# Kernel optimization log

Measured on AMD Instinct MI355X. Metric: run time of the kernel, lower is better.

## Reference

```python
import jax, jax.numpy as jnp
import numpy as np

N, E, DIN, DOUT = 30000, 480000, 512, 512


def setup_inputs() -> dict:
    key = jax.random.key(0)
    ks = jax.random.split(key, 20)
    inp = {}
    inp["x"] = jax.random.normal(ks[0], (N, DIN), jnp.float32)
    inp["edge_index"] = jax.random.randint(ks[1], (2, E), 0, N, dtype=jnp.int64)
    inp["edge_weight"] = jax.random.uniform(ks[2], (E,), jnp.float32)
    sc = 1.0 / np.sqrt(DIN)
    sl = 1.0 / np.sqrt(2 * DOUT)
    for i, g in enumerate(["i", "f", "g", "o"]):
        inp[f"Wc_{g}"] = jax.random.normal(ks[3 + 4 * i], (DIN, DOUT), jnp.float32) * sc
        inp[f"bc_{g}"] = jnp.zeros((DOUT,), jnp.float32)
        inp[f"Wl_{g}"] = jax.random.normal(ks[4 + 4 * i], (2 * DOUT, DOUT), jnp.float32) * sl
        inp[f"bl_{g}"] = jnp.zeros((DOUT,), jnp.float32)
    return inp


def _gcn_norm(src, dst, w, n):
    # add self loops with weight 1.0 (improved=False), then symmetric normalization
    loops = jnp.arange(n, dtype=src.dtype)
    src = jnp.concatenate([src, loops])
    dst = jnp.concatenate([dst, loops])
    w = jnp.concatenate([w, jnp.ones((n,), w.dtype)])
    deg = jax.ops.segment_sum(w, dst, num_segments=n)
    dinv = jnp.where(deg > 0, jax.lax.rsqrt(jnp.where(deg > 0, deg, 1.0)), 0.0)
    norm = dinv[src] * w * dinv[dst]
    return src, dst, norm


def reference(x, edge_index, edge_weight,
              Wc_i, bc_i, Wl_i, bl_i,
              Wc_f, bc_f, Wl_f, bl_f,
              Wc_g, bc_g, Wl_g, bl_g,
              Wc_o, bc_o, Wl_o, bl_o):
    n = x.shape[0]
    src, dst, norm = _gcn_norm(edge_index[0], edge_index[1], edge_weight, n)
    H = jnp.zeros((n, DOUT), x.dtype)  # _set_hidden_state default
    C = jnp.zeros((n, DOUT), x.dtype)  # _set_cell_state default

    def conv(Wc, bc):
        xw = x @ Wc                                        # [N, DOUT] dense GEMM
        agg = jax.ops.segment_sum(norm[:, None] * xw[src], dst, num_segments=n)
        return agg + bc

    def gate(Wc, bc, Wl, bl, act):
        z = jnp.concatenate([conv(Wc, bc), H], axis=1)      # [N, 2*DOUT]
        return act(z @ Wl + bl)

    I = gate(Wc_i, bc_i, Wl_i, bl_i, jax.nn.sigmoid)
    F = gate(Wc_f, bc_f, Wl_f, bl_f, jax.nn.sigmoid)
    G = gate(Wc_g, bc_g, Wl_g, bl_g, jnp.tanh)
    O = gate(Wc_o, bc_o, Wl_o, bl_o, jax.nn.sigmoid)
    Cn = F * C + I * G
    Hn = O * jnp.tanh(Cn)
    return O, Hn, Cn
```

## Files before the change

### kernel.cpp

```cpp
#include <hip/hip_runtime.h>
#include <stdint.h>

typedef __bf16 bf16;
typedef __attribute__((ext_vector_type(4))) float f4;
typedef __attribute__((ext_vector_type(4))) float f32x4;
typedef __attribute__((ext_vector_type(8))) __bf16 bf8v;
typedef __attribute__((ext_vector_type(4))) __bf16 bf4v;

#define NN 30000
#define MPAD 30080
#define OUTSTRIDE 15360000

typedef __attribute__((address_space(3))) unsigned int as3_u32;
typedef __attribute__((address_space(1))) unsigned int as1_u32;

__device__ __forceinline__ void gl_lds16(const void* g, void* l) {
  __builtin_amdgcn_global_load_lds((as1_u32*)g, (as3_u32*)l, 16, 0, 0);
}

__global__ void k_init(float* deg, int* counts, int* cursor, int n) {
  int i = blockIdx.x * 256 + threadIdx.x;
  if (i < n) { deg[i] = 1.0f; counts[i] = 0; cursor[i] = 0; }
}

__global__ void k_pre(const int* __restrict__ ei, const float* __restrict__ ew,
                      float* __restrict__ deg, int* __restrict__ counts, int E) {
  int e = blockIdx.x * 256 + threadIdx.x;
  if (e < E) {
    int d = ei[E + e];
    atomicAdd(&deg[d], ew[e]);
    atomicAdd(&counts[d], 1);
  }
}

__global__ void k_dinv(float* dinv, int n) {
  int i = blockIdx.x * 256 + threadIdx.x;
  if (i < n) { float d = dinv[i]; dinv[i] = d > 0.f ? rsqrtf(d) : 0.f; }
}

__global__ void k_bsum(const int* __restrict__ counts, int* __restrict__ bsum, int n) {
  __shared__ int sm[256];
  int i = blockIdx.x * 256 + threadIdx.x;
  sm[threadIdx.x] = (i < n) ? counts[i] : 0;
  __syncthreads();
  for (int st = 128; st > 0; st >>= 1) {
    if (threadIdx.x < st) sm[threadIdx.x] += sm[threadIdx.x + st];
    __syncthreads();
  }
  if (threadIdx.x == 0) bsum[blockIdx.x] = sm[0];
}

__global__ void k_bscan(int* bsum, int nb) {
  __shared__ int buf[128];
  int t = threadIdx.x;
  int v = (t < nb) ? bsum[t] : 0;
  buf[t] = v;
  __syncthreads();
  for (int s = 1; s < 128; s <<= 1) {
    int u = (t >= s) ? buf[t - s] : 0;
    __syncthreads();
    buf[t] += u;
    __syncthreads();
  }
  if (t < nb) bsum[t] = buf[t] - v;
}

__global__ void k_offs(const int* __restrict__ counts, const int* __restrict__ bsum,
                       int* __restrict__ offs, int n, int E) {
  __shared__ int buf[256];
  int i = blockIdx.x * 256 + threadIdx.x;
  int v = (i < n) ? counts[i] : 0;
  buf[threadIdx.x] = v;
  __syncthreads();
  for (int s = 1; s < 256; s <<= 1) {
    int u = (threadIdx.x >= s) ? buf[threadIdx.x - s] : 0;
    __syncthreads();
    buf[threadIdx.x] += u;
    __syncthreads();
  }
  if (i < n) offs[i] = bsum[blockIdx.x] + buf[threadIdx.x] - v;
  if (i == 0) offs[n] = E;
}

__global__ void k_scatter(const int* __restrict__ ei, const float* __restrict__ ew,
                          const float* __restrict__ dinv, const int* __restrict__ offs,
                          int* __restrict__ cursor, int* __restrict__ srcs,
                          float* __restrict__ norms, int E) {
  int e = blockIdx.x * 256 + threadIdx.x;
  if (e >= E) return;
  int s = ei[e], d = ei[E + e];
  int pos = offs[d] + atomicAdd(&cursor[d], 1);
  srcs[pos] = s;
  norms[pos] = dinv[s] * ew[e] * dinv[d];
}

__global__ void k_xbf(const float* __restrict__ x, bf16* __restrict__ xbf, int n8) {
  int i = blockIdx.x * 256 + threadIdx.x;
  if (i >= n8) return;
  const f4* x4 = (const f4*)x;
  f4 a = x4[2 * i], b = x4[2 * i + 1];
  bf8v o;
#pragma unroll
  for (int j = 0; j < 4; ++j) { o[j] = (bf16)a[j]; o[4 + j] = (bf16)b[j]; }
  ((bf8v*)xbf)[i] = o;
}

__global__ __launch_bounds__(256) void k_agg(const int* __restrict__ offs, const int* __restrict__ srcs,
                                             const float* __restrict__ norms, const float* __restrict__ x,
                                             const float* __restrict__ dinv, const bf16* __restrict__ xbf,
                                             bf16* __restrict__ ybf) {
  int wv = (blockIdx.x * 256 + threadIdx.x) >> 6;
  int lane = threadIdx.x & 63;
  if (wv >= MPAD) return;
  bf16* yrow = ybf + ((size_t)wv << 9) + lane * 8;
  if (wv >= NN) {
    bf8v z;
#pragma unroll
    for (int j = 0; j < 8; ++j) z[j] = (bf16)0.f;
    *(bf8v*)yrow = z;
    return;
  }
  float acc[8];
  float s0 = dinv[wv]; s0 *= s0;
  const f4* xr = (const f4*)(x + ((size_t)wv << 9)) + lane * 2;
  f4 a = xr[0], b = xr[1];
#pragma unroll
  for (int j = 0; j < 4; ++j) { acc[j] = s0 * a[j]; acc[4 + j] = s0 * b[j]; }
  int e = offs[wv], end = offs[wv + 1];
  for (; e + 2 <= end; e += 2) {
    int s1 = srcs[e], s2 = srcs[e + 1];
    float n1 = norms[e], n2 = norms[e + 1];
    bf8v v1 = *(const bf8v*)(xbf + ((size_t)s1 << 9) + lane * 8);
    bf8v v2 = *(const bf8v*)(xbf + ((size_t)s2 << 9) + lane * 8);
#pragma unroll
    for (int j = 0; j < 8; ++j) acc[j] += n1 * (float)v1[j] + n2 * (float)v2[j];
  }
  if (e < end) {
    int s1 = srcs[e]; float n1 = norms[e];
    bf8v v1 = *(const bf8v*)(xbf + ((size_t)s1 << 9) + lane * 8);
#pragma unroll
    for (int j = 0; j < 8; ++j) acc[j] += n1 * (float)v1[j];
  }
  bf8v o;
#pragma unroll
  for (int j = 0; j < 8; ++j) o[j] = (bf16)acc[j];
  *(bf8v*)yrow = o;
}

__global__ void k_wcomb(const float* __restrict__ WcA, const float* __restrict__ WlA,
                        const float* __restrict__ WcB, const float* __restrict__ WlB,
                        const float* __restrict__ WcC, const float* __restrict__ WlC,
                        bf16* __restrict__ Wt) {
  const float* Wc; const float* Wl;
  int g = blockIdx.z;
  if (g == 0)      { Wc = WcA; Wl = WlA; }
  else if (g == 1) { Wc = WcB; Wl = WlB; }
  else             { Wc = WcC; Wl = WlC; }
  int k0 = blockIdx.x * 64, j0 = blockIdx.y * 64;
  int t = threadIdx.x, tx = t & 15, ty = t >> 4;
  __shared__ float sWc[64][17];
  __shared__ float sWl[16][64];
  float acc[4][4] = {};
  for (int c0 = 0; c0 < 512; c0 += 16) {
    { int kk = t >> 2, c4 = (t & 3) * 4;
      f4 v = *(const f4*)(Wc + (size_t)(k0 + kk) * 512 + c0 + c4);
#pragma unroll
      for (int j = 0; j < 4; ++j) sWc[kk][c4 + j] = v[j]; }
    { int cc = t >> 4, j4 = (t & 15) * 4;
      f4 v = *(const f4*)(Wl + (size_t)(c0 + cc) * 512 + j0 + j4);
      *(f4*)&sWl[cc][j4] = v; }
    __syncthreads();
#pragma unroll
    for (int cc = 0; cc < 16; ++cc) {
      float wcv[4], wlv[4];
#pragma unroll
      for (int b = 0; b < 4; ++b) wcv[b] = sWc[tx * 4 + b][cc];
#pragma unroll
      for (int a = 0; a < 4; ++a) wlv[a] = sWl[cc][ty * 4 + a];
#pragma unroll
      for (int a = 0; a < 4; ++a)
#pragma unroll
        for (int b = 0; b < 4; ++b) acc[a][b] += wlv[a] * wcv[b];
    }
    __syncthreads();
  }
#pragma unroll
  for (int a = 0; a < 4; ++a) {
    bf4v o;
#pragma unroll
    for (int b = 0; b < 4; ++b) o[b] = (bf16)acc[a][b];
    *(bf4v*)&Wt[((size_t)g * 512 + j0 + ty * 4 + a) * 512 + k0 + tx * 4] = o;
  }
}

__global__ void k_bcomb3(const float* __restrict__ bcA, const float* __restrict__ blA, const float* __restrict__ WlA,
                         const float* __restrict__ bcB, const float* __restrict__ blB, const float* __restrict__ WlB,
                         const float* __restrict__ bcC, const float* __restrict__ blC, const float* __restrict__ WlC,
                         float* __restrict__ bcomb) {
  int g = blockIdx.x >> 3, jc = blockIdx.x & 7;
  const float* bc; const float* bl; const float* Wl;
  if (g == 0)      { bc = bcA; bl = blA; Wl = WlA; }
  else if (g == 1) { bc = bcB; bl = blB; Wl = WlB; }
  else             { bc = bcC; bl = blC; Wl = WlC; }
  int jl = threadIdx.x & 63, part = threadIdx.x >> 6;
  int j = jc * 64 + jl;
  float s = 0.f;
  for (int c = part * 128; c < part * 128 + 128; ++c)
    s += bc[c] * Wl[(size_t)c * 512 + j];
  __shared__ float sm[4][64];
  sm[part][jl] = s;
  __syncthreads();
  if (part == 0)
    bcomb[g * 512 + j] = bl[j] + sm[0][jl] + sm[1][jl] + sm[2][jl] + sm[3][jl];
}

__global__ __launch_bounds__(256) void k_gemm(const bf16* __restrict__ A, const bf16* __restrict__ Bt,
                                              const float* __restrict__ bcomb, float* __restrict__ out) {
  __shared__ __align__(16) char lds[81920];
  const int t = threadIdx.x, lane = t & 63, w = t >> 6;
  const int wm = w >> 1, wn = w & 1;
  const int d = blockIdx.x;
  const int s = (d & 7) * 235 + (d >> 3);
  const int m0 = (s >> 3) * 128, n0 = (s & 7) * 64;
  const int l15 = lane & 15, lhi = lane >> 4;
  f32x4 acc[3][4][2] = {};

  auto stage = [&](char* base, int ks) {
    const int k0b = ks * 128;
#pragma unroll
    for (int it = 0; it < 4; ++it) {
      int P = (((it * 4 + w) << 6) | lane) << 4;
      int r = P >> 7;
      int wl = (P & 127) ^ ((r & 7) << 4);
      gl_lds16((const char*)A + (((size_t)(m0 + r)) << 10) + k0b + wl, base + P);
    }
#pragma unroll
    for (int it = 0; it < 6; ++it) {
      int flat = it * 4 + w;
      int g = flat >> 3, q = flat & 7;
      int P = ((q << 6) | lane) << 4;
      int n = P >> 7;
      int wl = (P & 127) ^ ((n & 7) << 4);
      gl_lds16((const char*)Bt + (((size_t)(g * 512 + n0 + n)) << 10) + k0b + wl,
               base + 16384 + g * 8192 + P);
    }
  };

  auto compute = [&](const char* base) {
#pragma unroll
    for (int kh = 0; kh < 2; ++kh) {
      bf8v af[4];
#pragma unroll
      for (int mi = 0; mi < 4; ++mi) {
        int r = wm * 64 + mi * 16 + l15;
        int off = (kh * 64 + lhi * 16) ^ ((r & 7) << 4);
        af[mi] = *(const bf8v*)(base + r * 128 + off);
      }
      bf8v bfr[3][2];
#pragma unroll
      for (int g = 0; g < 3; ++g)
#pragma unroll
        for (int ni = 0; ni < 2; ++ni) {
          int n = wn * 32 + ni * 16 + l15;
          int off = (kh * 64 + lhi * 16) ^ ((n & 7) << 4);
          bfr[g][ni] = *(const bf8v*)(base + 16384 + g * 8192 + n * 128 + off);
        }
#pragma unroll
      for (int g = 0; g < 3; ++g)
#pragma unroll
        for (int mi = 0; mi < 4; ++mi)
#pragma unroll
          for (int ni = 0; ni < 2; ++ni)
            acc[g][mi][ni] = __builtin_amdgcn_mfma_f32_16x16x32_bf16(bfr[g][ni], af[mi], acc[g][mi][ni], 0, 0, 0);
    }
  };

  stage(lds, 0);
  __syncthreads();
#pragma unroll
  for (int kp = 0; kp < 4; ++kp) {
    stage(lds + 40960, 2 * kp + 1);
    compute(lds);
    __syncthreads();
    if (kp < 3) stage(lds, 2 * kp + 2);
    compute(lds + 40960);
    __syncthreads();
  }

#pragma unroll
  for (int ni = 0; ni < 2; ++ni) {
    int nb = n0 + wn * 32 + ni * 16 + lhi * 4;
    f4 bI = *(const f4*)&bcomb[nb];
    f4 bG = *(const f4*)&bcomb[512 + nb];
    f4 bO = *(const f4*)&bcomb[1024 + nb];
#pragma unroll
    for (int mi = 0; mi < 4; ++mi) {
      int row = m0 + wm * 64 + mi * 16 + l15;
      if (row < NN) {
        f4 vO, vH, vC;
#pragma unroll
        for (int r = 0; r < 4; ++r) {
          float zi = acc[0][mi][ni][r] + bI[r];
          float zg = acc[1][mi][ni][r] + bG[r];
          float zo = acc[2][mi][ni][r] + bO[r];
          float I = 1.f / (1.f + __expf(-zi));
          float e2g = __expf(2.f * zg);
          float G = (e2g - 1.f) / (e2g + 1.f);
          float O = 1.f / (1.f + __expf(-zo));
          float Cn = I * G;
          float e2c = __expf(2.f * Cn);
          float tc = (e2c - 1.f) / (e2c + 1.f);
          vO[r] = O; vH[r] = O * tc; vC[r] = Cn;
        }
        size_t base = ((size_t)row << 9) + nb;
        *(f4*)&out[base] = vO;
        *(f4*)&out[OUTSTRIDE + base] = vH;
        *(f4*)&out[2 * OUTSTRIDE + base] = vC;
      }
    }
  }
}

extern "C" void kernel_launch(void* const* d_in, const int* in_sizes, int n_in,
                              void* d_out, int out_size, void* d_ws, size_t ws_size,
                              hipStream_t stream) {
  const float* x   = (const float*)d_in[0];
  const int*   ei  = (const int*)d_in[1];
  const float* ew  = (const float*)d_in[2];
  const float* Wc_i = (const float*)d_in[3];
  const float* bc_i = (const float*)d_in[4];
  const float* Wl_i = (const float*)d_in[5];
  const float* bl_i = (const float*)d_in[6];
  const float* Wc_g = (const float*)d_in[11];
  const float* bc_g = (const float*)d_in[12];
  const float* Wl_g = (const float*)d_in[13];
  const float* bl_g = (const float*)d_in[14];
  const float* Wc_o = (const float*)d_in[15];
  const float* bc_o = (const float*)d_in[16];
  const float* Wl_o = (const float*)d_in[17];
  const float* bl_o = (const float*)d_in[18];

  const int E = in_sizes[2];
  const int n = in_sizes[0] / 512;
  const int NB = (n + 255) / 256;

  char* ws = (char*)d_ws;
  bf16*  ybf   = (bf16*)ws;
  float* dinv  = (float*)(ws + 30801920);
  bf16*  Wt    = (bf16*)(ws + 30924800);
  float* bcomb = (float*)(ws + 32497664);
  int*   bsum  = (int*)(ws + 32503808);
  (void)ws_size;

  char* ob = (char*)d_out;
  float* out   = (float*)d_out;
  bf16*  xbf   = (bf16*)ob;
  int*   srcs  = (int*)(ob + 30720000);
  float* norms = (float*)(ob + 32640000);
  int*   cnts  = (int*)(ob + 34560000);
  int*   offs  = (int*)(ob + 34680000);
  int*   curs  = (int*)(ob + 34800016);
  (void)out_size; (void)n_in;

  k_init<<<NB, 256, 0, stream>>>(dinv, cnts, curs, n);
  k_pre<<<(E + 255) / 256, 256, 0, stream>>>(ei, ew, dinv, cnts, E);
  k_dinv<<<NB, 256, 0, stream>>>(dinv, n);
  k_bsum<<<NB, 256, 0, stream>>>(cnts, bsum, n);
  k_bscan<<<1, 128, 0, stream>>>(bsum, NB);
  k_offs<<<NB, 256, 0, stream>>>(cnts, bsum, offs, n, E);
  k_scatter<<<(E + 255) / 256, 256, 0, stream>>>(ei, ew, dinv, offs, curs, srcs, norms, E);
  k_xbf<<<(n * 512 / 8 + 255) / 256, 256, 0, stream>>>(x, xbf, n * 512 / 8);
  k_agg<<<(MPAD * 64 + 255) / 256, 256, 0, stream>>>(offs, srcs, norms, x, dinv, xbf, ybf);
  k_wcomb<<<dim3(8, 8, 3), 256, 0, stream>>>(Wc_i, Wl_i, Wc_g, Wl_g, Wc_o, Wl_o, Wt);
  k_bcomb3<<<24, 256, 0, stream>>>(bc_i, bl_i, Wl_i, bc_g, bl_g, Wl_g, bc_o, bl_o, Wl_o, bcomb);
  k_gemm<<<1880, 256, 0, stream>>>(ybf, Wt, bcomb, out);
}
```

Measured before the change: 326.8 us.

## Drop LDS staging in gate GEMM, fuse dinv into bsum, read bf16 self term

The gate GEMM no longer stages A/B tiles through double-buffered LDS with async global-to-LDS loads. Each wave instead loads its MFMA fragments directly from global memory, and launch bounds request 3 blocks per CU for higher occupancy. The separate dinv kernel is folded into the block-sum kernel to save a launch. The aggregation self-loop term now reads the bf16 copy of x instead of fp32, which halves that read but adds rounding error. Removing LDS sharing increases global/L2 traffic because tiles are reloaded per wave.

```diff
diff --git a/kernel.cpp b/kernel.cpp
--- a/kernel.cpp
+++ b/kernel.cpp
@@ -10,13 +10,6 @@
 #define NN 30000
 #define MPAD 30080
 #define OUTSTRIDE 15360000
-
-typedef __attribute__((address_space(3))) unsigned int as3_u32;
-typedef __attribute__((address_space(1))) unsigned int as1_u32;
-
-__device__ __forceinline__ void gl_lds16(const void* g, void* l) {
-  __builtin_amdgcn_global_load_lds((as1_u32*)g, (as3_u32*)l, 16, 0, 0);
-}
 
 __global__ void k_init(float* deg, int* counts, int* cursor, int n) {
   int i = blockIdx.x * 256 + threadIdx.x;
@@ -33,15 +26,12 @@
   }
 }
 
-__global__ void k_dinv(float* dinv, int n) {
-  int i = blockIdx.x * 256 + threadIdx.x;
-  if (i < n) { float d = dinv[i]; dinv[i] = d > 0.f ? rsqrtf(d) : 0.f; }
-}
-
-__global__ void k_bsum(const int* __restrict__ counts, int* __restrict__ bsum, int n) {
+__global__ void k_bsum(const int* __restrict__ counts, int* __restrict__ bsum,
+                       float* __restrict__ dinv, int n) {
   __shared__ int sm[256];
   int i = blockIdx.x * 256 + threadIdx.x;
   sm[threadIdx.x] = (i < n) ? counts[i] : 0;
+  if (i < n) { float d = dinv[i]; dinv[i] = d > 0.f ? rsqrtf(d) : 0.f; }
   __syncthreads();
   for (int st = 128; st > 0; st >>= 1) {
     if (threadIdx.x < st) sm[threadIdx.x] += sm[threadIdx.x + st];
@@ -106,7 +96,7 @@
 }
 
 __global__ __launch_bounds__(256) void k_agg(const int* __restrict__ offs, const int* __restrict__ srcs,
-                                             const float* __restrict__ norms, const float* __restrict__ x,
+                                             const float* __restrict__ norms,
                                              const float* __restrict__ dinv, const bf16* __restrict__ xbf,
                                              bf16* __restrict__ ybf) {
   int wv = (blockIdx.x * 256 + threadIdx.x) >> 6;
@@ -122,10 +112,9 @@
   }
   float acc[8];
   float s0 = dinv[wv]; s0 *= s0;
-  const f4* xr = (const f4*)(x + ((size_t)wv << 9)) + lane * 2;
-  f4 a = xr[0], b = xr[1];
-#pragma unroll
-  for (int j = 0; j < 4; ++j) { acc[j] = s0 * a[j]; acc[4 + j] = s0 * b[j]; }
+  bf8v xv0 = *(const bf8v*)(xbf + ((size_t)wv << 9) + lane * 8);
+#pragma unroll
+  for (int j = 0; j < 8; ++j) acc[j] = s0 * (float)xv0[j];
   int e = offs[wv], end = offs[wv + 1];
   for (; e + 2 <= end; e += 2) {
     int s1 = srcs[e], s2 = srcs[e + 1];
@@ -214,9 +203,8 @@
     bcomb[g * 512 + j] = bl[j] + sm[0][jl] + sm[1][jl] + sm[2][jl] + sm[3][jl];
 }
 
-__global__ __launch_bounds__(256) void k_gemm(const bf16* __restrict__ A, const bf16* __restrict__ Bt,
-                                              const float* __restrict__ bcomb, float* __restrict__ out) {
-  __shared__ __align__(16) char lds[81920];
+__global__ __launch_bounds__(256, 3) void k_gemm(const bf16* __restrict__ A, const bf16* __restrict__ Bt,
+                                                 const float* __restrict__ bcomb, float* __restrict__ out) {
   const int t = threadIdx.x, lane = t & 63, w = t >> 6;
   const int wm = w >> 1, wn = w & 1;
   const int d = blockIdx.x;
@@ -225,46 +213,29 @@
   const int l15 = lane & 15, lhi = lane >> 4;
   f32x4 acc[3][4][2] = {};
 
-  auto stage = [&](char* base, int ks) {
-    const int k0b = ks * 128;
-#pragma unroll
-    for (int it = 0; it < 4; ++it) {
-      int P = (((it * 4 + w) << 6) | lane) << 4;
-      int r = P >> 7;
-      int wl = (P & 127) ^ ((r & 7) << 4);
-      gl_lds16((const char*)A + (((size_t)(m0 + r)) << 10) + k0b + wl, base + P);
-    }
-#pragma unroll
-    for (int it = 0; it < 6; ++it) {
-      int flat = it * 4 + w;
-      int g = flat >> 3, q = flat & 7;
-      int P = ((q << 6) | lane) << 4;
-      int n = P >> 7;
-      int wl = (P & 127) ^ ((n & 7) << 4);
-      gl_lds16((const char*)Bt + (((size_t)(g * 512 + n0 + n)) << 10) + k0b + wl,
-               base + 16384 + g * 8192 + P);
-    }
-  };
-
-  auto compute = [&](const char* base) {
+  const char* ap[4];
+#pragma unroll
+  for (int mi = 0; mi < 4; ++mi)
+    ap[mi] = (const char*)A + (((size_t)(m0 + wm * 64 + mi * 16 + l15)) << 10) + lhi * 16;
+  const char* bp[3][2];
+#pragma unroll
+  for (int g = 0; g < 3; ++g)
+#pragma unroll
+    for (int ni = 0; ni < 2; ++ni)
+      bp[g][ni] = (const char*)Bt + (((size_t)(g * 512 + n0 + wn * 32 + ni * 16 + l15)) << 10) + lhi * 16;
+
+#pragma unroll
+  for (int ks = 0; ks < 8; ++ks) {
 #pragma unroll
     for (int kh = 0; kh < 2; ++kh) {
-      bf8v af[4];
-#pragma unroll
-      for (int mi = 0; mi < 4; ++mi) {
-        int r = wm * 64 + mi * 16 + l15;
-        int off = (kh * 64 + lhi * 16) ^ ((r & 7) << 4);
-        af[mi] = *(const bf8v*)(base + r * 128 + off);
-      }
-      bf8v bfr[3][2];
+      const int off = ks * 128 + kh * 64;
+      bf8v af[4], bfr[3][2];
+#pragma unroll
+      for (int mi = 0; mi < 4; ++mi) af[mi] = *(const bf8v*)(ap[mi] + off);
 #pragma unroll
       for (int g = 0; g < 3; ++g)
 #pragma unroll
-        for (int ni = 0; ni < 2; ++ni) {
-          int n = wn * 32 + ni * 16 + l15;
-          int off = (kh * 64 + lhi * 16) ^ ((n & 7) << 4);
-          bfr[g][ni] = *(const bf8v*)(base + 16384 + g * 8192 + n * 128 + off);
-        }
+        for (int ni = 0; ni < 2; ++ni) bfr[g][ni] = *(const bf8v*)(bp[g][ni] + off);
 #pragma unroll
       for (int g = 0; g < 3; ++g)
 #pragma unroll
@@ -273,18 +244,6 @@
           for (int ni = 0; ni < 2; ++ni)
             acc[g][mi][ni] = __builtin_amdgcn_mfma_f32_16x16x32_bf16(bfr[g][ni], af[mi], acc[g][mi][ni], 0, 0, 0);
     }
-  };
-
-  stage(lds, 0);
-  __syncthreads();
-#pragma unroll
-  for (int kp = 0; kp < 4; ++kp) {
-    stage(lds + 40960, 2 * kp + 1);
-    compute(lds);
-    __syncthreads();
-    if (kp < 3) stage(lds, 2 * kp + 2);
-    compute(lds + 40960);
-    __syncthreads();
   }
 
 #pragma unroll
@@ -364,13 +323,12 @@
 
   k_init<<<NB, 256, 0, stream>>>(dinv, cnts, curs, n);
   k_pre<<<(E + 255) / 256, 256, 0, stream>>>(ei, ew, dinv, cnts, E);
-  k_dinv<<<NB, 256, 0, stream>>>(dinv, n);
-  k_bsum<<<NB, 256, 0, stream>>>(cnts, bsum, n);
+  k_bsum<<<NB, 256, 0, stream>>>(cnts, bsum, dinv, n);
   k_bscan<<<1, 128, 0, stream>>>(bsum, NB);
   k_offs<<<NB, 256, 0, stream>>>(cnts, bsum, offs, n, E);
   k_scatter<<<(E + 255) / 256, 256, 0, stream>>>(ei, ew, dinv, offs, curs, srcs, norms, E);
   k_xbf<<<(n * 512 / 8 + 255) / 256, 256, 0, stream>>>(x, xbf, n * 512 / 8);
-  k_agg<<<(MPAD * 64 + 255) / 256, 256, 0, stream>>>(offs, srcs, norms, x, dinv, xbf, ybf);
+  k_agg<<<(MPAD * 64 + 255) / 256, 256, 0, stream>>>(offs, srcs, norms, dinv, xbf, ybf);
   k_wcomb<<<dim3(8, 8, 3), 256, 0, stream>>>(Wc_i, Wl_i, Wc_g, Wl_g, Wc_o, Wl_o, Wt);
   k_bcomb3<<<24, 256, 0, stream>>>(bc_i, bl_i, Wl_i, bc_g, bl_g, Wl_g, bc_o, bl_o, Wl_o, bcomb);
   k_gemm<<<1880, 256, 0, stream>>>(ybf, Wt, bcomb, out);
```

New measurement: 393.2 us. 20.3% more time.
